# Performance work log

Hardware: AMD Instinct MI355X
Metric: run time of the kernel (lower is better)

The kernel has to match this reference:

```python
import jax, jax.numpy as jnp
import numpy as np

H = 512        # hidden_size
E = 512        # embedding_size
VOCAB = 32
OPS = 16
B = 64         # batch of trees
N = 1023       # complete binary tree, depth 9 (2^10 - 1 nodes)
TEMP = 3.0
INT_TYPES_MAX = 1  # types 0 (INT_PO) and 1 (INT_NE) carry a numeric arg


def setup_inputs() -> dict:
    key = jax.random.key(0)
    ks = jax.random.split(key, 12)
    s = 0.05
    return {
        "node_types": jax.random.randint(ks[0], (B, N), 0, VOCAB),
        "node_args": jax.random.normal(ks[1], (B, N), jnp.float32),
        "validity_mask": jax.random.uniform(ks[2], (B, OPS), jnp.float32, 1e-3, 1.0),
        "emb_table": jax.random.normal(ks[3], (VOCAB, E), jnp.float32) * s,
        "W_ih": jax.random.normal(ks[4], (8 * H, E), jnp.float32) * s,
        "W_hh": jax.random.normal(ks[5], (8 * H, 2 * H), jnp.float32) * s,
        "b_ih": jax.random.normal(ks[6], (8 * H,), jnp.float32) * s,
        "b_hh": jax.random.normal(ks[7], (8 * H,), jnp.float32) * s,
        "W1": jax.random.normal(ks[8], (H, H), jnp.float32) * s,
        "b1": jax.random.normal(ks[9], (H,), jnp.float32) * s,
        "W2": jax.random.normal(ks[10], (OPS, H), jnp.float32) * s,
        "b2": jax.random.normal(ks[11], (OPS,), jnp.float32) * s,
    }


def reference(node_types, node_args, validity_mask, emb_table,
              W_ih, W_hh, b_ih, b_hh, W1, b1, W2, b2):
    # --- SympleEmbedding: per-node embedding; int-typed nodes carry arg in last slot
    emb = emb_table[node_types]                                   # [B, N, E]
    is_int = node_types <= INT_TYPES_MAX                          # [B, N]
    emb = emb.at[..., -1].set(jnp.where(is_int, node_args, emb[..., -1]))

    # --- BinaryTreeLSTM, batched level-by-level (heap layout: children of i are 2i+1, 2i+2)
    D = int(np.log2(N + 1)) - 1                                   # depth of internal levels-1 = 9
    h = jnp.zeros((B, N, H), emb.dtype)                           # leaves: zeros
    c = jnp.zeros((B, N, H), emb.dtype)
    bias = b_ih + b_hh
    for d in range(D - 1, -1, -1):                                # bottom-up over internal levels
        idx = np.arange(2 ** d - 1, 2 ** (d + 1) - 1)             # nodes at level d
        left, right = 2 * idx + 1, 2 * idx + 2
        h0 = jnp.concatenate([h[:, left], h[:, right]], axis=-1)  # [B, n, 2H]
        c0 = jnp.concatenate([c[:, left], c[:, right]], axis=-1)
        gates = (jnp.einsum('bne,ge->bng', emb[:, idx], W_ih)
                 + jnp.einsum('bnh,gh->bng', h0, W_hh) + bias)    # [B, n, 8H]
        i_g, f_g, g_g, o_g = jnp.split(gates, 4, axis=-1)         # torch LSTM gate order i,f,g,o
        c_new = jax.nn.sigmoid(f_g) * c0 + jax.nn.sigmoid(i_g) * jnp.tanh(g_g)
        h_new = jax.nn.sigmoid(o_g) * jnp.tanh(c_new)
        h = h.at[:, idx].set(h_new[..., :H])                      # keep first H (as in module)
        c = c.at[:, idx].set(c_new[..., :H])

    # --- actor FFN on root hidden + validity-masked tempered softmax
    root_h = h[:, 0]                                              # [B, H]
    x = jax.nn.relu(root_h @ W1.T + b1)
    logits = x @ W2.T + b2 + jnp.log(validity_mask)
    return jax.nn.softmax(logits / TEMP, axis=-1)                 # [B, OPS]
```

## Files before the change

### kernel.cpp

```cpp
#include <hip/hip_runtime.h>
#include <math.h>

#define Nn 1023

typedef __attribute__((ext_vector_type(8))) short short8;
typedef __attribute__((ext_vector_type(4))) float f32x4;

#define AS1(p) ((const __attribute__((address_space(1))) void*)(p))
#define AS3(p) ((__attribute__((address_space(3))) void*)(p))

__device__ __forceinline__ float sigf(float x) { return 1.0f / (1.0f + __expf(-x)); }
__device__ __forceinline__ unsigned short f2bf(float x) {
    unsigned u = __float_as_uint(x);
    return (unsigned short)((u + 0x7fffu + ((u >> 16) & 1u)) >> 16);
}
__device__ __forceinline__ float bf2f(unsigned short b) {
    return __uint_as_float(((unsigned)b) << 16);
}

__global__ __launch_bounds__(256) void pack_whT(const float* __restrict__ W_hh,
                                                unsigned short* __restrict__ WhT) {
    int idx = blockIdx.x * 256 + threadIdx.x;
    int P = idx >> 7;
    int k0 = (idx & 127) * 8;
    int row = ((P >> 4) & 3) * 1024 + (P >> 6) * 16 + (P & 15);
    const float* src = W_hh + (size_t)row * 1024 + k0;
    float4 v0 = *(const float4*)src;
    float4 v1 = *(const float4*)(src + 4);
    short8 o;
    o[0] = (short)f2bf(v0.x); o[1] = (short)f2bf(v0.y);
    o[2] = (short)f2bf(v0.z); o[3] = (short)f2bf(v0.w);
    o[4] = (short)f2bf(v1.x); o[5] = (short)f2bf(v1.y);
    o[6] = (short)f2bf(v1.z); o[7] = (short)f2bf(v1.w);
    *(short8*)(WhT + (size_t)P * 1024 + k0) = o;
}

__global__ __launch_bounds__(256) void transpose512(const float* __restrict__ W1,
                                                    float* __restrict__ W1t) {
    __shared__ float tile[64][65];
    int jb = blockIdx.x * 64, kb = blockIdx.y * 64;
    int t = threadIdx.x;
    #pragma unroll
    for (int i = 0; i < 16; ++i) {
        int idx = t + i * 256;
        int lj = idx >> 6, lk = idx & 63;
        tile[lj][lk] = W1[(jb + lj) * 512 + kb + lk];
    }
    __syncthreads();
    #pragma unroll
    for (int i = 0; i < 16; ++i) {
        int idx = t + i * 256;
        int lk = idx >> 6, lj = idx & 63;
        W1t[(kb + lk) * 512 + jb + lj] = tile[lj][lk];
    }
}

__global__ __launch_bounds__(256) void prep_nodes(
    const int* __restrict__ node_types, const float* __restrict__ node_args,
    const float* __restrict__ emb, const float* __restrict__ W2,
    float* __restrict__ W2t, int* __restrict__ tyv, float* __restrict__ alphaf) {
    int gid = blockIdx.x * 256 + threadIdx.x;
    if (gid < 32704) {
        int node = gid >> 6, b = gid & 63;
        int ty = node_types[b * Nn + node];
        tyv[gid] = ty;
        alphaf[gid] = (ty <= 1) ? (node_args[b * Nn + node] - emb[ty * 512 + 511]) : 0.f;
    }
    if (gid < 8192) {
        int k = gid >> 4, op = gid & 15;
        W2t[gid] = W2[op * 512 + k];
    }
}

__global__ __launch_bounds__(256) void e32_kernel(
    const float* __restrict__ emb, const float* __restrict__ W_ih,
    const float* __restrict__ b_ih, const float* __restrict__ b_hh,
    float* __restrict__ E32b, float* __restrict__ w511f) {
    int o = blockIdx.x * 256 + threadIdx.x;
    int ty = o >> 11, P = o & 2047;
    int row = ((P >> 4) & 3) * 1024 + (P >> 6) * 16 + (P & 15);
    const float* er = emb + (size_t)ty * 512;
    const float* wr = W_ih + (size_t)row * 512;
    float s = b_ih[row] + b_hh[row];
    for (int k = 0; k < 512; k += 4) {
        float4 e4 = *(const float4*)(er + k);
        float4 w4 = *(const float4*)(wr + k);
        s = fmaf(e4.x, w4.x, fmaf(e4.y, w4.y, fmaf(e4.z, w4.z, fmaf(e4.w, w4.w, s))));
    }
    E32b[o] = s;
    if (ty == 0) w511f[P] = wr[511];
}

__global__ __launch_bounds__(256) void leaf_tables(
    const float* __restrict__ E32b,
    unsigned short* __restrict__ Hleaf, float* __restrict__ Cleaf) {
    int o = blockIdx.x * 256 + threadIdx.x;
    int ty = o >> 9, j = o & 511;
    int Pb = (j >> 4) * 64 + (j & 15);
    const float* Er = E32b + (size_t)ty * 2048;
    float ig = Er[Pb], gg = Er[Pb + 32], og = Er[Pb + 48];
    float cn = sigf(ig) * tanhf(gg);
    float hn = sigf(og) * tanhf(cn);
    Hleaf[o] = f2bf(hn);
    Cleaf[o] = cn;
}

__global__ __launch_bounds__(256) void leaf_int(
    const float* __restrict__ E32b, const float* __restrict__ w511f,
    const int* __restrict__ tyv, const float* __restrict__ alphaf,
    unsigned short* __restrict__ Hside, float* __restrict__ Cside) {
    int r = blockIdx.x * 4 + (threadIdx.x >> 6);
    int gn = 16320 + r;
    int ty = tyv[gn];
    if (ty > 1) return;
    float al = alphaf[gn];
    int l = r >> 6, b = r & 63;
    int jc = (threadIdx.x & 63) * 8;
    const float* Er = E32b + (size_t)ty * 2048;
    short8 hv;
    float cv[8];
    #pragma unroll
    for (int jj = 0; jj < 8; ++jj) {
        int j = jc + jj;
        int Pb = (j >> 4) * 64 + (j & 15);
        float ig = Er[Pb]      + al * w511f[Pb];
        float gg = Er[Pb + 32] + al * w511f[Pb + 32];
        float og = Er[Pb + 48] + al * w511f[Pb + 48];
        float cn = sigf(ig) * tanhf(gg);
        float hn = sigf(og) * tanhf(cn);
        hv[jj] = (short)f2bf(hn);
        cv[jj] = cn;
    }
    *(short8*)(Hside + (size_t)r * 512 + jc) = hv;
    if ((l & 1) == 0) {
        size_t cr = ((size_t)((l >> 1) * 64 + b)) * 512 + jc;
        float4 c0 = {cv[0], cv[1], cv[2], cv[3]};
        float4 c1 = {cv[4], cv[5], cv[6], cv[7]};
        *(float4*)(Cside + cr) = c0;
        *(float4*)(Cside + cr + 4) = c1;
    }
}

__global__ void zero_out(float* __restrict__ outp, int n) {
    int i = blockIdx.x * 256 + threadIdx.x;
    if (i < n) outp[i] = 0.f;
}

template<bool LEAFC>
__global__ __launch_bounds__(256) void lstm_mfma(
    const unsigned short* __restrict__ WhT, const float* __restrict__ E32b,
    const float* __restrict__ w511f,
    const int* __restrict__ tyv, const float* __restrict__ alphaf,
    const unsigned short* __restrict__ in_h, const float* __restrict__ in_c,
    const unsigned short* __restrict__ Hleaf, const unsigned short* __restrict__ Hside,
    const float* __restrict__ Cleaf, const float* __restrict__ Cside,
    unsigned short* __restrict__ out_h, float* __restrict__ out_c,
    int base, int nloc) {
    __shared__ __attribute__((aligned(16))) unsigned short AB[16384];
    unsigned short* As = AB;
    unsigned short* Bs = AB + 8192;
    const int t = threadIdx.x;
    const int w = t >> 6, lane = t & 63;
    const int wr = w >> 1, wc = w & 1;
    const int lane15 = lane & 15, lg = lane >> 4;
    const int M = nloc * 64;
    const int brow0 = blockIdx.x * 128;
    const int bcol0 = blockIdx.y * 128;
    const int lanek8 = (lane & 7) * 8;

    const unsigned short* baseL[4];
    const unsigned short* baseR[4];
    const unsigned short* wB[4];
    #pragma unroll
    for (int q = 0; q < 4; ++q) {
        int m = w * 32 + q * 8 + (lane >> 3);
        int r = brow0 + m; if (r > M - 1) r = M - 1;
        int lf = (r >> 6) * 128 + (r & 63);
        if (LEAFC) {
            int tyL = tyv[16320 + lf];
            int tyR = tyv[16320 + lf + 64];
            baseL[q] = (tyL <= 1) ? (Hside + (size_t)lf * 512)
                                  : (Hleaf + (size_t)tyL * 512);
            baseR[q] = (tyR <= 1) ? (Hside + (size_t)(lf + 64) * 512)
                                  : (Hleaf + (size_t)tyR * 512);
        } else {
            baseL[q] = in_h + (size_t)lf * 512;
            baseR[q] = baseL[q] + 64 * 512;
        }
        int P = bcol0 + w * 32 + q * 8 + (lane >> 3);
        wB[q] = WhT + (size_t)P * 1024;
    }

    f32x4 acc[4][4];
    float w4[4];
    int P4[4];
    #pragma unroll
    for (int q = 0; q < 4; ++q) {
        P4[q] = bcol0 + wc * 64 + q * 16 + lane15;
        w4[q] = w511f[P4[q]];
    }
    #pragma unroll
    for (int mi = 0; mi < 4; ++mi) {
        #pragma unroll
        for (int reg = 0; reg < 4; ++reg) {
            int r = brow0 + wr * 64 + mi * 16 + lg * 4 + reg;
            if (r > M - 1) r = M - 1;
            int gn = base * 64 + r;
            int ty = tyv[gn];
            float al = alphaf[gn];
            const float* Er = E32b + (size_t)ty * 2048;
            #pragma unroll
            for (int q = 0; q < 4; ++q)
                acc[mi][q][reg] = Er[P4[q]] + al * w4[q];
        }
    }

    for (int kt = 0; kt < 16; ++kt) {
        #pragma unroll
        for (int q = 0; q < 4; ++q) {
            const unsigned short* s = (kt < 8) ? (baseL[q] + kt * 64)
                                               : (baseR[q] + (kt - 8) * 64);
            __builtin_amdgcn_global_load_lds(AS1(s + lanek8),
                                             AS3(As + w * 2048 + q * 512), 16, 0, 0);
            __builtin_amdgcn_global_load_lds(AS1(wB[q] + kt * 64 + lanek8),
                                             AS3(Bs + w * 2048 + q * 512), 16, 0, 0);
        }
        __syncthreads();
        #pragma unroll
        for (int ks = 0; ks < 2; ++ks) {
            short8 av[4], bv[4];
            #pragma unroll
            for (int mi = 0; mi < 4; ++mi)
                av[mi] = *(const short8*)(As + (wr * 64 + mi * 16 + lane15) * 64 + ks * 32 + lg * 8);
            #pragma unroll
            for (int q = 0; q < 4; ++q)
                bv[q] = *(const short8*)(Bs + (wc * 64 + q * 16 + lane15) * 64 + ks * 32 + lg * 8);
            #pragma unroll
            for (int mi = 0; mi < 4; ++mi)
                #pragma unroll
                for (int q = 0; q < 4; ++q)
                    acc[mi][q] = __builtin_amdgcn_mfma_f32_16x16x32_bf16(av[mi], bv[q], acc[mi][q], 0, 0, 0);
        }
        __syncthreads();
    }

    const int j = (blockIdx.y * 2 + wc) * 16 + lane15;
    #pragma unroll
    for (int mi = 0; mi < 4; ++mi) {
        int rbase = brow0 + wr * 64 + mi * 16 + lg * 4;
        #pragma unroll
        for (int reg = 0; reg < 4; ++reg) {
            int r = rbase + reg;
            if (r < M) {
                float ig = acc[mi][0][reg];
                float fg = acc[mi][1][reg];
                float gg = acc[mi][2][reg];
                float og = acc[mi][3][reg];
                float cl;
                if (LEAFC) {
                    int lf = (r >> 6) * 128 + (r & 63);
                    int tyL = tyv[16320 + lf];
                    cl = (tyL <= 1) ? Cside[(size_t)r * 512 + j]
                                    : Cleaf[(size_t)tyL * 512 + j];
                } else {
                    cl = in_c[(size_t)r * 512 + j];
                }
                float cn = sigf(fg) * cl + sigf(ig) * tanhf(gg);
                float hn = sigf(og) * tanhf(cn);
                out_h[(size_t)r * 512 + j] = f2bf(hn);
                if (((r >> 6) & 1) == 0)
                    out_c[((size_t)((r >> 7) * 64 + (r & 63))) * 512 + j] = cn;
            }
        }
    }
}

__global__ __launch_bounds__(256) void head_kernel(
    const unsigned short* __restrict__ rootH, const float* __restrict__ W1t,
    const float* __restrict__ b1, const float* __restrict__ W2t,
    const float* __restrict__ b2, const float* __restrict__ vmask,
    float* __restrict__ outp) {
    __shared__ float rh[512];
    __shared__ float xs[512];
    __shared__ float part[16][17];
    int b = blockIdx.x, t = threadIdx.x;
    rh[t] = bf2f(rootH[b * 512 + t]);
    rh[t + 256] = bf2f(rootH[b * 512 + t + 256]);
    __syncthreads();
    #pragma unroll
    for (int jj = 0; jj < 2; ++jj) {
        int j = t + jj * 256;
        float acc = b1[j];
        for (int k = 0; k < 512; ++k) acc = fmaf(rh[k], W1t[k * 512 + j], acc);
        xs[j] = fmaxf(acc, 0.f);
    }
    __syncthreads();
    int op = t & 15, seg = t >> 4;
    float p = 0.f;
    for (int k = seg * 32; k < seg * 32 + 32; ++k) p = fmaf(xs[k], W2t[k * 16 + op], p);
    part[seg][op] = p;
    __syncthreads();
    if (t < 16) {
        float s = 0.f;
        #pragma unroll
        for (int g = 0; g < 16; ++g) s += part[g][t];
        float logit = s + b2[t] + logf(vmask[b * 16 + t]);
        float z = logit * (1.0f / 3.0f);
        float m = z;
        for (int off = 8; off; off >>= 1) m = fmaxf(m, __shfl_xor(m, off, 16));
        float e = __expf(z - m);
        float ssum = e;
        for (int off = 8; off; off >>= 1) ssum += __shfl_xor(ssum, off, 16);
        outp[b * 16 + t] = e / ssum;
    }
}

extern "C" void kernel_launch(void* const* d_in, const int* in_sizes, int n_in,
                              void* d_out, int out_size, void* d_ws, size_t ws_size,
                              hipStream_t stream) {
    const int*   node_types = (const int*)d_in[0];
    const float* node_args  = (const float*)d_in[1];
    const float* vmask      = (const float*)d_in[2];
    const float* emb_table  = (const float*)d_in[3];
    const float* W_ih       = (const float*)d_in[4];
    const float* W_hh       = (const float*)d_in[5];
    const float* b_ih       = (const float*)d_in[6];
    const float* b_hh       = (const float*)d_in[7];
    const float* W1         = (const float*)d_in[8];
    const float* b1         = (const float*)d_in[9];
    const float* W2         = (const float*)d_in[10];
    const float* b2         = (const float*)d_in[11];
    float* out = (float*)d_out;

    char* ws = (char*)d_ws;
    size_t off = 0;
    auto alloc = [&](size_t bytes) { char* p = ws + off; off += (bytes + 255) & ~(size_t)255; return p; };
    unsigned short* WhT  = (unsigned short*)alloc((size_t)2048 * 1024 * 2);
    float* E32b          = (float*)alloc((size_t)32 * 2048 * 4);
    float* w511f         = (float*)alloc(2048 * 4);
    float* W1t           = (float*)alloc((size_t)512 * 512 * 4);
    float* W2t           = (float*)alloc(8192 * 4);
    int*   tyv           = (int*)alloc(32704 * 4);
    float* alphaf        = (float*)alloc(32704 * 4);
    unsigned short* Hleaf= (unsigned short*)alloc((size_t)32 * 512 * 2);
    float* Cleaf         = (float*)alloc((size_t)32 * 512 * 4);
    unsigned short* Hside= (unsigned short*)alloc((size_t)16384 * 512 * 2);
    float* Cside         = (float*)alloc((size_t)8192 * 512 * 4);
    unsigned short* Xh   = (unsigned short*)alloc((size_t)8192 * 512 * 2);
    unsigned short* Yh   = (unsigned short*)alloc((size_t)4096 * 512 * 2);
    float* Xc            = (float*)alloc((size_t)4096 * 512 * 4);
    float* Yc            = (float*)alloc((size_t)2048 * 512 * 4);

    if (ws_size < off) {
        zero_out<<<(out_size + 255) / 256, 256, 0, stream>>>(out, out_size);
        return;
    }

    pack_whT<<<1024, 256, 0, stream>>>(W_hh, WhT);
    transpose512<<<dim3(8, 8), 256, 0, stream>>>(W1, W1t);
    prep_nodes<<<128, 256, 0, stream>>>(node_types, node_args, emb_table, W2, W2t, tyv, alphaf);
    e32_kernel<<<256, 256, 0, stream>>>(emb_table, W_ih, b_ih, b_hh, E32b, w511f);
    leaf_tables<<<64, 256, 0, stream>>>(E32b, Hleaf, Cleaf);
    leaf_int<<<4096, 256, 0, stream>>>(E32b, w511f, tyv, alphaf, Hside, Cside);

    lstm_mfma<true><<<dim3(64, 16), 256, 0, stream>>>(
        WhT, E32b, w511f, tyv, alphaf,
        nullptr, nullptr, Hleaf, Hside, Cleaf, Cside,
        Xh, Xc, 127, 128);

    for (int d = 6; d >= 0; --d) {
        int nloc = 1 << d;
        unsigned short* oh = (d & 1) ? Xh : Yh;
        float* oc          = (d & 1) ? Xc : Yc;
        const unsigned short* ih = (d & 1) ? Yh : Xh;
        const float* ic          = (d & 1) ? Yc : Xc;
        int gx = (nloc >= 2) ? (nloc / 2) : 1;
        lstm_mfma<false><<<dim3(gx, 16), 256, 0, stream>>>(
            WhT, E32b, w511f, tyv, alphaf, ih, ic,
            nullptr, nullptr, nullptr, nullptr,
            oh, oc, nloc - 1, nloc);
    }

    head_kernel<<<64, 256, 0, stream>>>(Yh, W1t, b1, W2t, b2, vmask, out);
}
```

Before: 444.2 us.

## Use per-type lookup tables for level 7 and compact int-child rows for MFMA

```diff
diff --git a/kernel.cpp b/kernel.cpp
--- a/kernel.cpp
+++ b/kernel.cpp
@@ -10,6 +10,10 @@
 #define AS3(p) ((__attribute__((address_space(3))) void*)(p))
 
 __device__ __forceinline__ float sigf(float x) { return 1.0f / (1.0f + __expf(-x)); }
+__device__ __forceinline__ float tanhfast(float x) {
+    float e = __expf(2.0f * x);
+    return 1.0f - 2.0f / (e + 1.0f);
+}
 __device__ __forceinline__ unsigned short f2bf(float x) {
     unsigned u = __float_as_uint(x);
     return (unsigned short)((u + 0x7fffu + ((u >> 16) & 1u)) >> 16);
@@ -93,15 +97,17 @@
 
 __global__ __launch_bounds__(256) void leaf_tables(
     const float* __restrict__ E32b,
-    unsigned short* __restrict__ Hleaf, float* __restrict__ Cleaf) {
+    unsigned short* __restrict__ Hleaf, float* __restrict__ Hleaf_f,
+    float* __restrict__ Cleaf) {
     int o = blockIdx.x * 256 + threadIdx.x;
     int ty = o >> 9, j = o & 511;
     int Pb = (j >> 4) * 64 + (j & 15);
     const float* Er = E32b + (size_t)ty * 2048;
     float ig = Er[Pb], gg = Er[Pb + 32], og = Er[Pb + 48];
-    float cn = sigf(ig) * tanhf(gg);
-    float hn = sigf(og) * tanhf(cn);
+    float cn = sigf(ig) * tanhfast(gg);
+    float hn = sigf(og) * tanhfast(cn);
     Hleaf[o] = f2bf(hn);
+    Hleaf_f[o] = hn;
     Cleaf[o] = cn;
 }
 
@@ -126,8 +132,8 @@
         float ig = Er[Pb]      + al * w511f[Pb];
         float gg = Er[Pb + 32] + al * w511f[Pb + 32];
         float og = Er[Pb + 48] + al * w511f[Pb + 48];
-        float cn = sigf(ig) * tanhf(gg);
-        float hn = sigf(og) * tanhf(cn);
+        float cn = sigf(ig) * tanhfast(gg);
+        float hn = sigf(og) * tanhfast(cn);
         hv[jj] = (short)f2bf(hn);
         cv[jj] = cn;
     }
@@ -141,12 +147,110 @@
     }
 }
 
+__global__ __launch_bounds__(256) void glgr_kernel(
+    const float* __restrict__ W_hh, const float* __restrict__ Hleaf_f,
+    float* __restrict__ GLt, float* __restrict__ GRt,
+    int* __restrict__ rowidx, int* __restrict__ cnt) {
+    int gid = blockIdx.x * 256 + threadIdx.x;
+    if (gid < 8448) rowidx[gid] = 0;
+    if (gid == 8448) *cnt = 0;
+    int side = gid >> 16, ty = (gid >> 11) & 31, P = gid & 2047;
+    int row = ((P >> 4) & 3) * 1024 + (P >> 6) * 16 + (P & 15);
+    const float* wr = W_hh + (size_t)row * 1024 + side * 512;
+    const float* hr = Hleaf_f + (size_t)ty * 512;
+    float s = 0.f;
+    for (int k = 0; k < 512; k += 4) {
+        float4 w4 = *(const float4*)(wr + k);
+        float4 h4 = *(const float4*)(hr + k);
+        s = fmaf(w4.x, h4.x, fmaf(w4.y, h4.y, fmaf(w4.z, h4.z, fmaf(w4.w, h4.w, s))));
+    }
+    if (side == 0) GLt[ty * 2048 + P] = s;
+    else           GRt[ty * 2048 + P] = s;
+}
+
+__global__ __launch_bounds__(256) void flag_k(
+    const int* __restrict__ tyv, int* __restrict__ rowidx, int* __restrict__ cnt) {
+    int r = blockIdx.x * 256 + threadIdx.x;
+    int lf = (r >> 6) * 128 + (r & 63);
+    if (tyv[16320 + lf] <= 1 || tyv[16320 + lf + 64] <= 1) {
+        int p = atomicAdd(cnt, 1);
+        rowidx[p] = r;
+    }
+}
+
 __global__ void zero_out(float* __restrict__ outp, int n) {
     int i = blockIdx.x * 256 + threadIdx.x;
     if (i < n) outp[i] = 0.f;
 }
 
-template<bool LEAFC>
+__global__ __launch_bounds__(256) void d7_table_cell(
+    const float* __restrict__ E32b, const float* __restrict__ GLt,
+    const float* __restrict__ GRt, const float* __restrict__ Cleaf,
+    const float* __restrict__ Cside, const float* __restrict__ w511f,
+    const int* __restrict__ tyv, const float* __restrict__ alphaf,
+    unsigned short* __restrict__ out_h, float* __restrict__ out_c) {
+    __shared__ float Es[32][129];
+    __shared__ float GLs[32][129];
+    __shared__ float GRs[32][129];
+    __shared__ float Cls[32][33];
+    __shared__ float w5s[128];
+    const int t = threadIdx.x;
+    const int j0 = blockIdx.y * 32;
+    const int r = blockIdx.x * 256 + t;
+
+    for (int i = t; i < 32 * 128; i += 256) {
+        int ty = i >> 7, pp = i & 127;
+        int gp = ((j0 >> 4) + (pp >> 6)) * 64 + (pp & 63);
+        Es[ty][pp]  = E32b[ty * 2048 + gp];
+        GLs[ty][pp] = GLt[ty * 2048 + gp];
+        GRs[ty][pp] = GRt[ty * 2048 + gp];
+    }
+    for (int i = t; i < 32 * 32; i += 256) {
+        int ty = i >> 5, jl = i & 31;
+        Cls[ty][jl] = Cleaf[ty * 512 + j0 + jl];
+    }
+    if (t < 128) w5s[t] = w511f[((j0 >> 4) + (t >> 6)) * 64 + (t & 63)];
+    __syncthreads();
+
+    int gn = 8128 + r;
+    int tyP = tyv[gn];
+    float aP = alphaf[gn];
+    int lf = (r >> 6) * 128 + (r & 63);
+    int tyL = tyv[16320 + lf];
+    int tyR = tyv[16320 + lf + 64];
+    bool intL = (tyL <= 1);
+    bool evenl = (((r >> 6) & 1) == 0);
+    size_t crow = ((size_t)((r >> 7) * 64 + (r & 63))) * 512;
+
+    #pragma unroll
+    for (int j8 = 0; j8 < 4; ++j8) {
+        short8 hv;
+        float cv[8];
+        #pragma unroll
+        for (int jj = 0; jj < 8; ++jj) {
+            int jl = j8 * 8 + jj;
+            int ppb = (jl >> 4) * 64 + (jl & 15);
+            float ig = Es[tyP][ppb]      + aP * w5s[ppb]      + GLs[tyL][ppb]      + GRs[tyR][ppb];
+            float fg = Es[tyP][ppb + 16] + aP * w5s[ppb + 16] + GLs[tyL][ppb + 16] + GRs[tyR][ppb + 16];
+            float gg = Es[tyP][ppb + 32] + aP * w5s[ppb + 32] + GLs[tyL][ppb + 32] + GRs[tyR][ppb + 32];
+            float og = Es[tyP][ppb + 48] + aP * w5s[ppb + 48] + GLs[tyL][ppb + 48] + GRs[tyR][ppb + 48];
+            float cl = intL ? Cside[(size_t)r * 512 + j0 + jl] : Cls[tyL][jl];
+            float cn = sigf(fg) * cl + sigf(ig) * tanhfast(gg);
+            float hn = sigf(og) * tanhfast(cn);
+            hv[jj] = (short)f2bf(hn);
+            cv[jj] = cn;
+        }
+        *(short8*)(out_h + (size_t)r * 512 + j0 + j8 * 8) = hv;
+        if (evenl) {
+            float4 c0 = {cv[0], cv[1], cv[2], cv[3]};
+            float4 c1 = {cv[4], cv[5], cv[6], cv[7]};
+            *(float4*)(out_c + crow + j0 + j8 * 8) = c0;
+            *(float4*)(out_c + crow + j0 + j8 * 8 + 4) = c1;
+        }
+    }
+}
+
+template<int MODE>
 __global__ __launch_bounds__(256) void lstm_mfma(
     const unsigned short* __restrict__ WhT, const float* __restrict__ E32b,
     const float* __restrict__ w511f,
@@ -154,11 +258,10 @@
     const unsigned short* __restrict__ in_h, const float* __restrict__ in_c,
     const unsigned short* __restrict__ Hleaf, const unsigned short* __restrict__ Hside,
     const float* __restrict__ Cleaf, const float* __restrict__ Cside,
+    const int* __restrict__ rowidx, const int* __restrict__ cnt,
     unsigned short* __restrict__ out_h, float* __restrict__ out_c,
     int base, int nloc) {
-    __shared__ __attribute__((aligned(16))) unsigned short AB[16384];
-    unsigned short* As = AB;
-    unsigned short* Bs = AB + 8192;
+    extern __shared__ unsigned short AB[];
     const int t = threadIdx.x;
     const int w = t >> 6, lane = t & 63;
     const int wr = w >> 1, wc = w & 1;
@@ -168,15 +271,23 @@
     const int bcol0 = blockIdx.y * 128;
     const int lanek8 = (lane & 7) * 8;
 
+    if (MODE == 2) {
+        int nc = *cnt;
+        int padded = (nc + 127) & ~127;
+        if (brow0 >= padded) return;
+    }
+
     const unsigned short* baseL[4];
     const unsigned short* baseR[4];
     const unsigned short* wB[4];
     #pragma unroll
     for (int q = 0; q < 4; ++q) {
         int m = w * 32 + q * 8 + (lane >> 3);
-        int r = brow0 + m; if (r > M - 1) r = M - 1;
+        int r = brow0 + m;
+        if (MODE == 2) r = rowidx[r];
+        else if (r > M - 1) r = M - 1;
         int lf = (r >> 6) * 128 + (r & 63);
-        if (LEAFC) {
+        if (MODE >= 1) {
             int tyL = tyv[16320 + lf];
             int tyR = tyv[16320 + lf + 64];
             baseL[q] = (tyL <= 1) ? (Hside + (size_t)lf * 512)
@@ -191,9 +302,26 @@
         wB[q] = WhT + (size_t)P * 1024;
     }
 
+    auto stage = [&](int kt, int cur) {
+        unsigned short* Ad = AB + cur * 16384;
+        unsigned short* Bd = Ad + 8192;
+        #pragma unroll
+        for (int q = 0; q < 4; ++q) {
+            const unsigned short* s = (kt < 8) ? (baseL[q] + kt * 64)
+                                               : (baseR[q] + (kt - 8) * 64);
+            __builtin_amdgcn_global_load_lds(AS1(s + lanek8),
+                                             AS3(Ad + w * 2048 + q * 512), 16, 0, 0);
+            __builtin_amdgcn_global_load_lds(AS1(wB[q] + kt * 64 + lanek8),
+                                             AS3(Bd + w * 2048 + q * 512), 16, 0, 0);
+        }
+    };
+
+    stage(0, 0);
+
     f32x4 acc[4][4];
     float w4[4];
     int P4[4];
+    int rr[4][4];
     #pragma unroll
     for (int q = 0; q < 4; ++q) {
         P4[q] = bcol0 + wc * 64 + q * 16 + lane15;
@@ -204,7 +332,9 @@
         #pragma unroll
         for (int reg = 0; reg < 4; ++reg) {
             int r = brow0 + wr * 64 + mi * 16 + lg * 4 + reg;
-            if (r > M - 1) r = M - 1;
+            if (MODE == 2) r = rowidx[r];
+            else if (r > M - 1) r = M - 1;
+            rr[mi][reg] = r;
             int gn = base * 64 + r;
             int ty = tyv[gn];
             float al = alphaf[gn];
@@ -215,49 +345,43 @@
         }
     }
 
+    int cur = 0;
     for (int kt = 0; kt < 16; ++kt) {
-        #pragma unroll
-        for (int q = 0; q < 4; ++q) {
-            const unsigned short* s = (kt < 8) ? (baseL[q] + kt * 64)
-                                               : (baseR[q] + (kt - 8) * 64);
-            __builtin_amdgcn_global_load_lds(AS1(s + lanek8),
-                                             AS3(As + w * 2048 + q * 512), 16, 0, 0);
-            __builtin_amdgcn_global_load_lds(AS1(wB[q] + kt * 64 + lanek8),
-                                             AS3(Bs + w * 2048 + q * 512), 16, 0, 0);
-        }
         __syncthreads();
+        if (kt < 15) stage(kt + 1, cur ^ 1);
+        const unsigned short* Ac = AB + cur * 16384;
+        const unsigned short* Bc = Ac + 8192;
         #pragma unroll
         for (int ks = 0; ks < 2; ++ks) {
             short8 av[4], bv[4];
             #pragma unroll
             for (int mi = 0; mi < 4; ++mi)
-                av[mi] = *(const short8*)(As + (wr * 64 + mi * 16 + lane15) * 64 + ks * 32 + lg * 8);
+                av[mi] = *(const short8*)(Ac + (wr * 64 + mi * 16 + lane15) * 64 + ks * 32 + lg * 8);
             #pragma unroll
             for (int q = 0; q < 4; ++q)
-                bv[q] = *(const short8*)(Bs + (wc * 64 + q * 16 + lane15) * 64 + ks * 32 + lg * 8);
+                bv[q] = *(const short8*)(Bc + (wc * 64 + q * 16 + lane15) * 64 + ks * 32 + lg * 8);
             #pragma unroll
             for (int mi = 0; mi < 4; ++mi)
                 #pragma unroll
                 for (int q = 0; q < 4; ++q)
                     acc[mi][q] = __builtin_amdgcn_mfma_f32_16x16x32_bf16(av[mi], bv[q], acc[mi][q], 0, 0, 0);
         }
-        __syncthreads();
+        cur ^= 1;
     }
 
     const int j = (blockIdx.y * 2 + wc) * 16 + lane15;
     #pragma unroll
     for (int mi = 0; mi < 4; ++mi) {
-        int rbase = brow0 + wr * 64 + mi * 16 + lg * 4;
         #pragma unroll
         for (int reg = 0; reg < 4; ++reg) {
-            int r = rbase + reg;
+            int r = rr[mi][reg];
             if (r < M) {
                 float ig = acc[mi][0][reg];
                 float fg = acc[mi][1][reg];
                 float gg = acc[mi][2][reg];
                 float og = acc[mi][3][reg];
                 float cl;
-                if (LEAFC) {
+                if (MODE >= 1) {
                     int lf = (r >> 6) * 128 + (r & 63);
                     int tyL = tyv[16320 + lf];
                     cl = (tyL <= 1) ? Cside[(size_t)r * 512 + j]
@@ -265,8 +389,8 @@
                 } else {
                     cl = in_c[(size_t)r * 512 + j];
                 }
-                float cn = sigf(fg) * cl + sigf(ig) * tanhf(gg);
-                float hn = sigf(og) * tanhf(cn);
+                float cn = sigf(fg) * cl + sigf(ig) * tanhfast(gg);
+                float hn = sigf(og) * tanhfast(cn);
                 out_h[(size_t)r * 512 + j] = f2bf(hn);
                 if (((r >> 6) & 1) == 0)
                     out_c[((size_t)((r >> 7) * 64 + (r & 63))) * 512 + j] = cn;
@@ -343,7 +467,12 @@
     int*   tyv           = (int*)alloc(32704 * 4);
     float* alphaf        = (float*)alloc(32704 * 4);
     unsigned short* Hleaf= (unsigned short*)alloc((size_t)32 * 512 * 2);
+    float* Hleaf_f       = (float*)alloc((size_t)32 * 512 * 4);
     float* Cleaf         = (float*)alloc((size_t)32 * 512 * 4);
+    float* GLt           = (float*)alloc((size_t)32 * 2048 * 4);
+    float* GRt           = (float*)alloc((size_t)32 * 2048 * 4);
+    int*   rowidx        = (int*)alloc(8448 * 4);
+    int*   cnt           = (int*)alloc(256);
     unsigned short* Hside= (unsigned short*)alloc((size_t)16384 * 512 * 2);
     float* Cside         = (float*)alloc((size_t)8192 * 512 * 4);
     unsigned short* Xh   = (unsigned short*)alloc((size_t)8192 * 512 * 2);
@@ -360,13 +489,17 @@
     transpose512<<<dim3(8, 8), 256, 0, stream>>>(W1, W1t);
     prep_nodes<<<128, 256, 0, stream>>>(node_types, node_args, emb_table, W2, W2t, tyv, alphaf);
     e32_kernel<<<256, 256, 0, stream>>>(emb_table, W_ih, b_ih, b_hh, E32b, w511f);
-    leaf_tables<<<64, 256, 0, stream>>>(E32b, Hleaf, Cleaf);
+    leaf_tables<<<64, 256, 0, stream>>>(E32b, Hleaf, Hleaf_f, Cleaf);
     leaf_int<<<4096, 256, 0, stream>>>(E32b, w511f, tyv, alphaf, Hside, Cside);
-
-    lstm_mfma<true><<<dim3(64, 16), 256, 0, stream>>>(
+    glgr_kernel<<<512, 256, 0, stream>>>(W_hh, Hleaf_f, GLt, GRt, rowidx, cnt);
+    flag_k<<<32, 256, 0, stream>>>(tyv, rowidx, cnt);
+
+    d7_table_cell<<<dim3(32, 16), 256, 0, stream>>>(
+        E32b, GLt, GRt, Cleaf, Cside, w511f, tyv, alphaf, Xh, Xc);
+    lstm_mfma<2><<<dim3(64, 16), 256, 65536, stream>>>(
         WhT, E32b, w511f, tyv, alphaf,
         nullptr, nullptr, Hleaf, Hside, Cleaf, Cside,
-        Xh, Xc, 127, 128);
+        rowidx, cnt, Xh, Xc, 127, 128);
 
     for (int d = 6; d >= 0; --d) {
         int nloc = 1 << d;
@@ -375,10 +508,10 @@
         const unsigned short* ih = (d & 1) ? Yh : Xh;
         const float* ic          = (d & 1) ? Yc : Xc;
         int gx = (nloc >= 2) ? (nloc / 2) : 1;
-        lstm_mfma<false><<<dim3(gx, 16), 256, 0, stream>>>(
+        lstm_mfma<0><<<dim3(gx, 16), 256, 65536, stream>>>(
             WhT, E32b, w511f, tyv, alphaf, ih, ic,
             nullptr, nullptr, nullptr, nullptr,
-            oh, oc, nloc - 1, nloc);
+            nullptr, nullptr, oh, oc, nloc - 1, nloc);
     }
 
     head_kernel<<<64, 256, 0, stream>>>(Yh, W1t, b1, W2t, b2, vmask, out);
```

Result: faster. 420.0 us (-5.4%).
